# Optimization experiments

Hardware: AMD Instinct MI355X
Metric: run time of the kernel (lower is better)

The kernel has to match this reference:

```python
import jax, jax.numpy as jnp
import numpy as np

BN_EPS = 1e-5


def setup_inputs() -> dict:
    key = jax.random.key(0)
    k1, k2, k3 = jax.random.split(key, 3)
    B, C, H, W = 8, 1024, 48, 48
    Cb = 512
    x = jax.random.normal(k1, (B, C, H, W), dtype=jnp.float32)
    Wg = jax.random.normal(k2, (Cb, C), dtype=jnp.float32) * (1.0 / np.sqrt(C))
    Wz = jax.random.normal(k3, (C, Cb), dtype=jnp.float32) * (1.0 / np.sqrt(Cb))
    gamma = jnp.zeros((C,), dtype=jnp.float32)  # BN weight, const-init 0
    beta = jnp.zeros((C,), dtype=jnp.float32)   # BN bias,  const-init 0
    return {"x": x, "Wg": Wg, "Wz": Wz, "gamma": gamma, "beta": beta}


def reference(x, Wg, Wz, gamma, beta):
    B, C, H, W = x.shape
    HW = H * W
    xf = x.reshape(B, C, HW)                                  # [B,C,N]
    # attn[b,n,m] = <x[b,:,n], x[b,:,m]> / (H*W), softmax over m
    attn = jnp.einsum('bcn,bcm->bnm', xf, xf) / HW            # [B,N,N]
    attn = jax.nn.softmax(attn, axis=-1)
    # g: 1x1 conv C -> Cb (no bias)
    g = jnp.einsum('dc,bcn->bdn', Wg, xf)                     # [B,Cb,N]
    # y[b,d,n] = sum_m attn[b,n,m] * g[b,d,m]
    y = jnp.einsum('bnm,bdm->bdn', attn, g)                   # [B,Cb,N]
    # W_z: 1x1 conv Cb -> C (no bias)
    wy = jnp.einsum('cd,bdn->bcn', Wz, y)                     # [B,C,N]
    # BatchNorm2d in training mode: batch stats over (B, N), biased variance
    mean = jnp.mean(wy, axis=(0, 2), keepdims=True)
    var = jnp.mean(jnp.square(wy - mean), axis=(0, 2), keepdims=True)
    wy_bn = (wy - mean) * jax.lax.rsqrt(var + BN_EPS)
    wy_bn = wy_bn * gamma[None, :, None] + beta[None, :, None]
    z = wy_bn.reshape(B, C, H, W) + x
    return z
```

## Files before the change

### kernel.cpp

```cpp
#include <hip/hip_runtime.h>
#include <hip/hip_bf16.h>
#include <stdint.h>


typedef __bf16 bf16;
typedef __attribute__((ext_vector_type(8))) __bf16 bf16x8;
typedef __attribute__((ext_vector_type(4))) float f32x4;

template <bool F32OUT, bool BNRED>
__global__ __launch_bounds__(256)
void gemm_bt(const bf16* __restrict__ Ag, const bf16* __restrict__ Bg,
             void* __restrict__ Dg, int K, int N,
             long long sA, long long sB, long long sD, float alpha,
             float* __restrict__ ps, float* __restrict__ pq)
{
    __shared__ char lds[32768];
    char* ldsA = lds;
    char* ldsB = lds + 16384;

    const int lane = threadIdx.x & 63;
    const int wv   = threadIdx.x >> 6;
    const int wm   = wv >> 1;
    const int wn   = wv & 1;

    const bf16* Ab = Ag + (long long)blockIdx.z * sA + (long long)blockIdx.y * 128 * K;
    const bf16* Bb = Bg + (long long)blockIdx.z * sB + (long long)blockIdx.x * 128 * K;

    f32x4 acc[4][4];
    #pragma unroll
    for (int i = 0; i < 4; ++i)
        #pragma unroll
        for (int j = 0; j < 4; ++j) {
            f32x4 z = {0.f, 0.f, 0.f, 0.f};
            acc[i][j] = z;
        }

    for (int k0 = 0; k0 < K; k0 += 64) {
        #pragma unroll
        for (int t = 0; t < 4; ++t) {
            int ch  = (wv * 4 + t) * 64 + lane;
            int row = ch >> 3;
            int cc  = (ch & 7) ^ (row & 7);
            bf16x8 va = *(const bf16x8*)(Ab + (long long)row * K + k0 + cc * 8);
            bf16x8 vb = *(const bf16x8*)(Bb + (long long)row * K + k0 + cc * 8);
            *(bf16x8*)(ldsA + ch * 16) = va;
            *(bf16x8*)(ldsB + ch * 16) = vb;
        }
        __syncthreads();

        #pragma unroll
        for (int kk = 0; kk < 64; kk += 32) {
            bf16x8 af[4], bfr[4];
            #pragma unroll
            for (int i = 0; i < 4; ++i) {
                int r = wm * 64 + i * 16 + (lane & 15);
                int c = ((kk >> 3) + (lane >> 4)) ^ (r & 7);
                af[i] = *(const bf16x8*)(ldsA + r * 128 + c * 16);
            }
            #pragma unroll
            for (int j = 0; j < 4; ++j) {
                int r = wn * 64 + j * 16 + (lane & 15);
                int c = ((kk >> 3) + (lane >> 4)) ^ (r & 7);
                bfr[j] = *(const bf16x8*)(ldsB + r * 128 + c * 16);
            }
            #pragma unroll
            for (int i = 0; i < 4; ++i)
                #pragma unroll
                for (int j = 0; j < 4; ++j)
                    acc[i][j] = __builtin_amdgcn_mfma_f32_16x16x32_bf16(af[i], bfr[j], acc[i][j], 0, 0, 0);
        }
        __syncthreads();
    }

    float* bs = (float*)lds;
    float* bq = (float*)(lds + 512);
    if (BNRED) {
        if (threadIdx.x < 128) { bs[threadIdx.x] = 0.f; bq[threadIdx.x] = 0.f; }
        __syncthreads();
    }

    const int m_base = blockIdx.y * 128 + wm * 64;
    const int n_base = blockIdx.x * 128 + wn * 64;
    float s_it[4][4], q_it[4][4];
    #pragma unroll
    for (int i = 0; i < 4; ++i) {
        #pragma unroll
        for (int t = 0; t < 4; ++t) { s_it[i][t] = 0.f; q_it[i][t] = 0.f; }
    }
    #pragma unroll
    for (int i = 0; i < 4; ++i) {
        #pragma unroll
        for (int j = 0; j < 4; ++j) {
            int col = n_base + j * 16 + (lane & 15);
            #pragma unroll
            for (int t = 0; t < 4; ++t) {
                int rowg = m_base + i * 16 + (lane >> 4) * 4 + t;
                float v = acc[i][j][t] * alpha;
                if (F32OUT) ((float*)Dg)[(long long)blockIdx.z * sD + (long long)rowg * N + col] = v;
                else        ((bf16*)Dg)[(long long)blockIdx.z * sD + (long long)rowg * N + col] = (bf16)v;
                if (BNRED) { s_it[i][t] += v; q_it[i][t] += v * v; }
            }
        }
    }

    if (BNRED) {
        #pragma unroll
        for (int i = 0; i < 4; ++i) {
            #pragma unroll
            for (int t = 0; t < 4; ++t) {
                float s = s_it[i][t], q = q_it[i][t];
                #pragma unroll
                for (int m = 1; m < 16; m <<= 1) {
                    s += __shfl_xor(s, m);
                    q += __shfl_xor(q, m);
                }
                if ((lane & 15) == 0) {
                    int cl = wm * 64 + i * 16 + (lane >> 4) * 4 + t;
                    atomicAdd(&bs[cl], s);
                    atomicAdd(&bq[cl], q);
                }
            }
        }
        __syncthreads();
        if (threadIdx.x < 128) {
            int cg = blockIdx.y * 128 + threadIdx.x;
            atomicAdd(&ps[cg], bs[threadIdx.x]);
            atomicAdd(&pq[cg], bq[threadIdx.x]);
        }
    }
}

__global__ __launch_bounds__(256)
void f32_to_bf16(const float* __restrict__ in, bf16* __restrict__ out, int n)
{
    int idx = (blockIdx.x * 256 + threadIdx.x) * 4;
    if (idx < n) {
        float4 v = *(const float4*)(in + idx);
        out[idx + 0] = (bf16)v.x;
        out[idx + 1] = (bf16)v.y;
        out[idx + 2] = (bf16)v.z;
        out[idx + 3] = (bf16)v.w;
    }
}

__global__ __launch_bounds__(256)
void zero_f32(float* __restrict__ p)
{
    p[blockIdx.x * 256 + threadIdx.x] = 0.f;
}

__global__ __launch_bounds__(256)
void transpose_f32_bf16(const float* __restrict__ x, bf16* __restrict__ xT)
{
    __shared__ bf16 tile[32][33];
    const float* xb = x + (long long)blockIdx.z * 1024 * 2304;
    bf16* xo = xT + (long long)blockIdx.z * 2304 * 1024;
    const int n0 = blockIdx.x * 32;
    const int c0 = blockIdx.y * 32;
    const int tx = threadIdx.x, ty = threadIdx.y;
    #pragma unroll
    for (int i = 0; i < 32; i += 8)
        tile[ty + i][tx] = (bf16)xb[(long long)(c0 + ty + i) * 2304 + n0 + tx];
    __syncthreads();
    #pragma unroll
    for (int i = 0; i < 32; i += 8)
        xo[(long long)(n0 + ty + i) * 1024 + c0 + tx] = tile[tx][ty + i];
}

__global__ __launch_bounds__(256)
void softmax_rows(bf16* __restrict__ S)
{
    bf16* p = S + (long long)blockIdx.x * 2304;
    const int t = threadIdx.x;
    __shared__ float red[256];

    bf16x8 v8 = *(const bf16x8*)(p + t * 8);
    float vt = (float)p[2048 + t];
    float f[8];
    float mx = vt;
    #pragma unroll
    for (int i = 0; i < 8; ++i) { f[i] = (float)v8[i]; mx = fmaxf(mx, f[i]); }

    red[t] = mx; __syncthreads();
    for (int s = 128; s > 0; s >>= 1) { if (t < s) red[t] = fmaxf(red[t], red[t + s]); __syncthreads(); }
    mx = red[0];
    __syncthreads();

    float sum = 0.f;
    #pragma unroll
    for (int i = 0; i < 8; ++i) { f[i] = __expf(f[i] - mx); sum += f[i]; }
    vt = __expf(vt - mx); sum += vt;

    red[t] = sum; __syncthreads();
    for (int s = 128; s > 0; s >>= 1) { if (t < s) red[t] += red[t + s]; __syncthreads(); }
    float inv = 1.0f / red[0];

    bf16x8 o;
    #pragma unroll
    for (int i = 0; i < 8; ++i) o[i] = (bf16)(f[i] * inv);
    *(bf16x8*)(p + t * 8) = o;
    p[2048 + t] = (bf16)(vt * inv);
}

__global__ __launch_bounds__(256)
void bn_finalize(const float* __restrict__ ps, const float* __restrict__ pq,
                 float* __restrict__ mean, float* __restrict__ istd)
{
    int c = blockIdx.x * 256 + threadIdx.x;
    float mu = ps[c] / 18432.0f;
    mean[c] = mu;
    istd[c] = rsqrtf(pq[c] / 18432.0f - mu * mu + 1e-5f);
}

__global__ __launch_bounds__(256)
void bn_apply(const float* __restrict__ wy, const float* __restrict__ x,
              const float* __restrict__ gamma, const float* __restrict__ beta,
              const float* __restrict__ mean, const float* __restrict__ istd,
              float* __restrict__ z)
{
    long long idx = ((long long)blockIdx.x * 256 + threadIdx.x) * 4;
    int c = (int)((idx / 2304) & 1023);
    float sc = gamma[c] * istd[c];
    float sh = beta[c] - mean[c] * sc;
    float4 w  = *(const float4*)(wy + idx);
    float4 xv = *(const float4*)(x + idx);
    float4 o;
    o.x = w.x * sc + sh + xv.x;
    o.y = w.y * sc + sh + xv.y;
    o.z = w.z * sc + sh + xv.z;
    o.w = w.w * sc + sh + xv.w;
    *(float4*)(z + idx) = o;
}

extern "C" void kernel_launch(void* const* d_in, const int* in_sizes, int n_in,
                              void* d_out, int out_size, void* d_ws, size_t ws_size,
                              hipStream_t stream)
{
    const float* x     = (const float*)d_in[0];
    const float* Wg    = (const float*)d_in[1];
    const float* Wz    = (const float*)d_in[2];
    const float* gamma = (const float*)d_in[3];
    const float* beta  = (const float*)d_in[4];
    float* zo = (float*)d_out;

    const int B = 8, C = 1024, Cb = 512, N = 2304;

    const size_t fixedB = ((size_t)Cb * C * 2) * 2 + (size_t)C * 4 * 4 + 4096;
    const size_t perB   = ((size_t)N * C + (size_t)Cb * N + (size_t)N * N + (size_t)N * Cb) * 2 + 1024;
    int BC = 8;
    while (BC > 1 && fixedB + perB * (size_t)BC > ws_size) BC >>= 1;

    char* p = (char*)d_ws;
    auto alloc = [&](size_t bytes) { char* r = p; p += (bytes + 255) & ~(size_t)255; return r; };
    bf16*  Wgb  = (bf16*)alloc((size_t)Cb * C * 2);
    bf16*  Wzb  = (bf16*)alloc((size_t)C * Cb * 2);
    float* psum = (float*)alloc((size_t)C * 4);
    float* pqsm = (float*)alloc((size_t)C * 4);
    float* mean = (float*)alloc((size_t)C * 4);
    float* istd = (float*)alloc((size_t)C * 4);
    bf16*  xT   = (bf16*)alloc((size_t)BC * N * C * 2);
    bf16*  g    = (bf16*)alloc((size_t)BC * Cb * N * 2);
    bf16*  attn = (bf16*)alloc((size_t)BC * N * N * 2);
    bf16*  yT   = (bf16*)alloc((size_t)BC * N * Cb * 2);

    f32_to_bf16<<<dim3((Cb * C) / (256 * 4)), 256, 0, stream>>>(Wg, Wgb, Cb * C);
    f32_to_bf16<<<dim3((C * Cb) / (256 * 4)), 256, 0, stream>>>(Wz, Wzb, C * Cb);
    zero_f32<<<dim3(8), 256, 0, stream>>>(psum);

    for (int cs = 0; cs < B; cs += BC) {
        const float* xc = x + (long long)cs * C * N;
        float* wyc = zo + (long long)cs * C * N;

        transpose_f32_bf16<<<dim3(N / 32, C / 32, BC), dim3(32, 8), 0, stream>>>(xc, xT);

        gemm_bt<false, false><<<dim3(N / 128, Cb / 128, BC), 256, 0, stream>>>(
            Wgb, xT, g, C, N, 0, (long long)N * C, (long long)Cb * N, 1.0f, nullptr, nullptr);

        gemm_bt<false, false><<<dim3(N / 128, N / 128, BC), 256, 0, stream>>>(
            xT, xT, attn, C, N, (long long)N * C, (long long)N * C, (long long)N * N, 1.0f / 2304.0f,
            nullptr, nullptr);

        softmax_rows<<<dim3(BC * N), 256, 0, stream>>>(attn);

        gemm_bt<false, false><<<dim3(Cb / 128, N / 128, BC), 256, 0, stream>>>(
            attn, g, yT, N, Cb, (long long)N * N, (long long)Cb * N, (long long)N * Cb, 1.0f,
            nullptr, nullptr);

        gemm_bt<true, true><<<dim3(N / 128, C / 128, BC), 256, 0, stream>>>(
            Wzb, yT, wyc, Cb, N, 0, (long long)N * Cb, (long long)C * N, 1.0f, psum, pqsm);
    }

    bn_finalize<<<dim3(C / 256), 256, 0, stream>>>(psum, pqsm, mean, istd);
    bn_apply<<<dim3((B * C * N) / (256 * 4)), 256, 0, stream>>>(zo, x, gamma, beta, mean, istd, zo);
}
```

Before: 445.0 us.

## Add 256x256-tile 8-wave GEMM with double-buffered LDS pipeline for bf16 GEMMs

Adds a new bf16 GEMM kernel using 256x256 output tiles with 512 threads, XOR-swizzled LDS, a 128-wide K step split into phases, register-staged global prefetch into a double-buffered 128KB LDS, and s_setprio around MFMA bursts. It replaces the 128x128 kernel for the g, attention and attn*g GEMMs. The larger tiles are meant to raise arithmetic intensity and overlap global loads with MFMA work. In exchange they reduce grid size, which may hurt occupancy and CU fill for the smaller GEMMs. They also need heavy LDS and register use and assume dimensions divisible by 256.

New measurement: 458.3 us. 3.0% more time.

```diff
diff --git a/kernel.cpp b/kernel.cpp
--- a/kernel.cpp
+++ b/kernel.cpp
@@ -6,6 +6,157 @@
 typedef __bf16 bf16;
 typedef __attribute__((ext_vector_type(8))) __bf16 bf16x8;
 typedef __attribute__((ext_vector_type(4))) float f32x4;
+
+__device__ __forceinline__ void wg_barrier()
+{
+    asm volatile("" ::: "memory");
+    __builtin_amdgcn_s_barrier();
+    asm volatile("" ::: "memory");
+}
+
+__global__ __launch_bounds__(512, 2)
+void gemm_bt256(const bf16* __restrict__ Ag, const bf16* __restrict__ Bg,
+                bf16* __restrict__ Dg, int K, int N,
+                long long sA, long long sB, long long sD, float alpha)
+{
+    __shared__ __align__(16) char lds[131072];
+
+    const int tid  = threadIdx.x;
+    const int lane = tid & 63;
+    const int wv   = tid >> 6;
+    const int wm   = wv >> 2;
+    const int wn   = wv & 3;
+
+    const bf16* Ab = Ag + (long long)blockIdx.z * sA + (long long)blockIdx.y * 256 * K;
+    const bf16* Bb = Bg + (long long)blockIdx.z * sB + (long long)blockIdx.x * 256 * K;
+
+    const int r0 = tid >> 3,        c0 = (tid & 7) ^ (r0 & 7);
+    const int r1 = (tid + 512) >> 3, c1 = (tid & 7) ^ (r1 & 7);
+    auto gofs0 = [&](int half, int kb) { return (half * 128 + r0) * K + kb + c0 * 8; };
+    auto gofs1 = [&](int half, int kb) { return (half * 128 + r1) * K + kb + c1 * 8; };
+
+    const int NIT = K >> 7;
+
+    static constexpr int  srcB[8] = {1, 1, 0, 0, 1, 1, 0, 0};
+    static constexpr int  half[8] = {0, 1, 0, 1, 0, 1, 0, 1};
+    static constexpr int  kof [8] = {128, 128, 128, 128, 192, 192, 192, 192};
+    static constexpr int  wof [8] = {98304, 114688, 65536, 81920, 32768, 49152, 0, 16384};
+
+    f32x4 acc[8][4];
+    #pragma unroll
+    for (int i = 0; i < 8; ++i)
+        #pragma unroll
+        for (int j = 0; j < 4; ++j) {
+            f32x4 z = {0.f, 0.f, 0.f, 0.f};
+            acc[i][j] = z;
+        }
+
+    bf16x8 sl[4][2];
+    bf16x8 bfrag[4][2];
+
+    {
+        bf16x8 b0a = *(const bf16x8*)(Bb + gofs0(0, 0));
+        bf16x8 b0b = *(const bf16x8*)(Bb + gofs1(0, 0));
+        bf16x8 b1a = *(const bf16x8*)(Bb + gofs0(1, 0));
+        bf16x8 b1b = *(const bf16x8*)(Bb + gofs1(1, 0));
+        bf16x8 a0a = *(const bf16x8*)(Ab + gofs0(0, 0));
+        bf16x8 a0b = *(const bf16x8*)(Ab + gofs1(0, 0));
+        bf16x8 a1a = *(const bf16x8*)(Ab + gofs0(1, 0));
+        bf16x8 a1b = *(const bf16x8*)(Ab + gofs1(1, 0));
+        sl[0][0] = *(const bf16x8*)(Bb + gofs0(0, 64));
+        sl[0][1] = *(const bf16x8*)(Bb + gofs1(0, 64));
+        sl[1][0] = *(const bf16x8*)(Bb + gofs0(1, 64));
+        sl[1][1] = *(const bf16x8*)(Bb + gofs1(1, 64));
+        sl[2][0] = *(const bf16x8*)(Ab + gofs0(0, 64));
+        sl[2][1] = *(const bf16x8*)(Ab + gofs1(0, 64));
+        sl[3][0] = *(const bf16x8*)(Ab + gofs0(1, 64));
+        sl[3][1] = *(const bf16x8*)(Ab + gofs1(1, 64));
+        *(bf16x8*)(lds + 32768 + tid * 16) = b0a;
+        *(bf16x8*)(lds + 40960 + tid * 16) = b0b;
+        *(bf16x8*)(lds + 49152 + tid * 16) = b1a;
+        *(bf16x8*)(lds + 57344 + tid * 16) = b1b;
+        *(bf16x8*)(lds + 0     + tid * 16) = a0a;
+        *(bf16x8*)(lds + 8192  + tid * 16) = a0b;
+        *(bf16x8*)(lds + 16384 + tid * 16) = a1a;
+        *(bf16x8*)(lds + 24576 + tid * 16) = a1b;
+        asm volatile("s_waitcnt lgkmcnt(0)" ::: "memory");
+        wg_barrier();
+        __builtin_amdgcn_sched_barrier(0);
+    }
+
+    for (int it = 0; it < NIT; ++it) {
+        const int kc = it << 7;
+        const bool pf = (it + 1 < NIT);
+        #pragma unroll
+        for (int p = 0; p < 8; ++p) {
+            const int d = p >> 2, q = p & 3, s = p & 3;
+            char* dA = lds + d * 65536;
+            char* dB = dA + 32768;
+
+            if (q == 0) {
+                #pragma unroll
+                for (int j = 0; j < 4; ++j) {
+                    int r = wn * 64 + j * 16 + (lane & 15);
+                    #pragma unroll
+                    for (int ks = 0; ks < 2; ++ks) {
+                        int c = ((ks * 4) + (lane >> 4)) ^ (r & 7);
+                        bfrag[j][ks] = *(const bf16x8*)(dB + r * 128 + c * 16);
+                    }
+                }
+            }
+            bf16x8 af[2][2];
+            #pragma unroll
+            for (int ii = 0; ii < 2; ++ii) {
+                int r = wm * 128 + (q * 2 + ii) * 16 + (lane & 15);
+                #pragma unroll
+                for (int ks = 0; ks < 2; ++ks) {
+                    int c = ((ks * 4) + (lane >> 4)) ^ (r & 7);
+                    af[ii][ks] = *(const bf16x8*)(dA + r * 128 + c * 16);
+                }
+            }
+
+            if (p < 4 || pf) {
+                *(bf16x8*)(lds + wof[p] + tid * 16)        = sl[s][0];
+                *(bf16x8*)(lds + wof[p] + 8192 + tid * 16) = sl[s][1];
+            }
+            if (pf) {
+                const bf16* src = srcB[p] ? Bb : Ab;
+                sl[s][0] = *(const bf16x8*)(src + gofs0(half[p], kc + kof[p]));
+                sl[s][1] = *(const bf16x8*)(src + gofs1(half[p], kc + kof[p]));
+            }
+
+            wg_barrier();
+            asm volatile("s_waitcnt lgkmcnt(0)" ::: "memory");
+            __builtin_amdgcn_s_setprio(1);
+            #pragma unroll
+            for (int ks = 0; ks < 2; ++ks)
+                #pragma unroll
+                for (int ii = 0; ii < 2; ++ii)
+                    #pragma unroll
+                    for (int j = 0; j < 4; ++j)
+                        acc[q * 2 + ii][j] = __builtin_amdgcn_mfma_f32_16x16x32_bf16(
+                            af[ii][ks], bfrag[j][ks], acc[q * 2 + ii][j], 0, 0, 0);
+            __builtin_amdgcn_s_setprio(0);
+            wg_barrier();
+            __builtin_amdgcn_sched_barrier(0);
+        }
+    }
+
+    const int m_base = blockIdx.y * 256 + wm * 128;
+    const int n_base = blockIdx.x * 256 + wn * 64;
+    bf16* Db = Dg + (long long)blockIdx.z * sD;
+    #pragma unroll
+    for (int i = 0; i < 8; ++i)
+        #pragma unroll
+        for (int j = 0; j < 4; ++j) {
+            int col = n_base + j * 16 + (lane & 15);
+            #pragma unroll
+            for (int t = 0; t < 4; ++t) {
+                int rowg = m_base + i * 16 + (lane >> 4) * 4 + t;
+                Db[(long long)rowg * N + col] = (bf16)(acc[i][j][t] * alpha);
+            }
+        }
+}
 
 template <bool F32OUT, bool BNRED>
 __global__ __launch_bounds__(256)
@@ -273,18 +424,17 @@
 
         transpose_f32_bf16<<<dim3(N / 32, C / 32, BC), dim3(32, 8), 0, stream>>>(xc, xT);
 
-        gemm_bt<false, false><<<dim3(N / 128, Cb / 128, BC), 256, 0, stream>>>(
-            Wgb, xT, g, C, N, 0, (long long)N * C, (long long)Cb * N, 1.0f, nullptr, nullptr);
-
-        gemm_bt<false, false><<<dim3(N / 128, N / 128, BC), 256, 0, stream>>>(
-            xT, xT, attn, C, N, (long long)N * C, (long long)N * C, (long long)N * N, 1.0f / 2304.0f,
-            nullptr, nullptr);
+        gemm_bt256<<<dim3(N / 256, Cb / 256, BC), 512, 0, stream>>>(
+            Wgb, xT, g, C, N, 0, (long long)N * C, (long long)Cb * N, 1.0f);
+
+        gemm_bt256<<<dim3(N / 256, N / 256, BC), 512, 0, stream>>>(
+            xT, xT, attn, C, N, (long long)N * C, (long long)N * C, (long long)N * N,
+            1.0f / 2304.0f);
 
         softmax_rows<<<dim3(BC * N), 256, 0, stream>>>(attn);
 
-        gemm_bt<false, false><<<dim3(Cb / 128, N / 128, BC), 256, 0, stream>>>(
-            attn, g, yT, N, Cb, (long long)N * N, (long long)Cb * N, (long long)N * Cb, 1.0f,
-            nullptr, nullptr);
+        gemm_bt256<<<dim3(Cb / 256, N / 256, BC), 512, 0, stream>>>(
+            attn, g, yT, N, Cb, (long long)N * N, (long long)Cb * N, (long long)N * Cb, 1.0f);
 
         gemm_bt<true, true><<<dim3(N / 128, C / 128, BC), 256, 0, stream>>>(
             Wzb, yT, wyc, Cb, N, 0, (long long)N * Cb, (long long)C * N, 1.0f, psum, pqsm);
```

## Exploit symmetry of x^T x to compute only upper-triangular attention tiles

Applied to the files above, without the earlier changes.

Replaces the attention-score GEMM with a kernel that computes only tiles on or above the diagonal, since x^T x is symmetric. Off-diagonal tiles also write their transpose through an LDS staging buffer, and diagonal tiles load the operand only once. This roughly halves the matmul work for the largest GEMM. In exchange, half the launched blocks exit immediately, scalar LDS transpose writes are added, and LDS use grows slightly.

After: 436.0 us. 1.02x faster.

```diff
diff --git a/kernel.cpp b/kernel.cpp
--- a/kernel.cpp
+++ b/kernel.cpp
@@ -131,6 +131,105 @@
 }
 
 __global__ __launch_bounds__(256)
+void gemm_sym(const bf16* __restrict__ Xg, bf16* __restrict__ Dg,
+              int K, int N, long long sX, long long sD, float alpha)
+{
+    const int bi = blockIdx.y, bj = blockIdx.x;
+    if (bj < bi) return;
+    const bool mir  = (bj > bi);
+    const bool diag = (bj == bi);
+
+    __shared__ __align__(16) char lds[34816];
+    char* ldsA = lds;
+    char* ldsB = diag ? lds : (lds + 16384);
+
+    const int lane = threadIdx.x & 63;
+    const int wv   = threadIdx.x >> 6;
+    const int wm   = wv >> 1;
+    const int wn   = wv & 1;
+
+    const bf16* Ab = Xg + (long long)blockIdx.z * sX + (long long)bi * 128 * K;
+    const bf16* Bb = Xg + (long long)blockIdx.z * sX + (long long)bj * 128 * K;
+
+    f32x4 acc[4][4];
+    #pragma unroll
+    for (int i = 0; i < 4; ++i)
+        #pragma unroll
+        for (int j = 0; j < 4; ++j) {
+            f32x4 z = {0.f, 0.f, 0.f, 0.f};
+            acc[i][j] = z;
+        }
+
+    for (int k0 = 0; k0 < K; k0 += 64) {
+        #pragma unroll
+        for (int t = 0; t < 4; ++t) {
+            int ch  = (wv * 4 + t) * 64 + lane;
+            int row = ch >> 3;
+            int cc  = (ch & 7) ^ (row & 7);
+            bf16x8 va = *(const bf16x8*)(Ab + (long long)row * K + k0 + cc * 8);
+            *(bf16x8*)(ldsA + ch * 16) = va;
+            if (!diag) {
+                bf16x8 vb = *(const bf16x8*)(Bb + (long long)row * K + k0 + cc * 8);
+                *(bf16x8*)(ldsB + ch * 16) = vb;
+            }
+        }
+        __syncthreads();
+
+        #pragma unroll
+        for (int kk = 0; kk < 64; kk += 32) {
+            bf16x8 af[4], bfr[4];
+            #pragma unroll
+            for (int i = 0; i < 4; ++i) {
+                int r = wm * 64 + i * 16 + (lane & 15);
+                int c = ((kk >> 3) + (lane >> 4)) ^ (r & 7);
+                af[i] = *(const bf16x8*)(ldsA + r * 128 + c * 16);
+            }
+            #pragma unroll
+            for (int j = 0; j < 4; ++j) {
+                int r = wn * 64 + j * 16 + (lane & 15);
+                int c = ((kk >> 3) + (lane >> 4)) ^ (r & 7);
+                bfr[j] = *(const bf16x8*)(ldsB + r * 128 + c * 16);
+            }
+            #pragma unroll
+            for (int i = 0; i < 4; ++i)
+                #pragma unroll
+                for (int j = 0; j < 4; ++j)
+                    acc[i][j] = __builtin_amdgcn_mfma_f32_16x16x32_bf16(af[i], bfr[j], acc[i][j], 0, 0, 0);
+        }
+        __syncthreads();
+    }
+
+    bf16* Db = Dg + (long long)blockIdx.z * sD;
+    bf16 (*tr)[136] = (bf16(*)[136])lds;
+
+    #pragma unroll
+    for (int i = 0; i < 4; ++i) {
+        #pragma unroll
+        for (int j = 0; j < 4; ++j) {
+            int c_loc = wn * 64 + j * 16 + (lane & 15);
+            int col   = bj * 128 + c_loc;
+            #pragma unroll
+            for (int t = 0; t < 4; ++t) {
+                int r_loc = wm * 64 + i * 16 + (lane >> 4) * 4 + t;
+                float v = acc[i][j][t] * alpha;
+                Db[(long long)(bi * 128 + r_loc) * N + col] = (bf16)v;
+                if (mir) tr[c_loc][r_loc] = (bf16)v;
+            }
+        }
+    }
+
+    if (mir) {
+        __syncthreads();
+        const int cc = threadIdx.x >> 1, hf = threadIdx.x & 1;
+        const bf16* src = &tr[cc][hf * 64];
+        bf16* dst = Db + (long long)(bj * 128 + cc) * N + bi * 128 + hf * 64;
+        #pragma unroll
+        for (int j2 = 0; j2 < 8; ++j2)
+            *(bf16x8*)(dst + j2 * 8) = *(const bf16x8*)(src + j2 * 8);
+    }
+}
+
+__global__ __launch_bounds__(256)
 void f32_to_bf16(const float* __restrict__ in, bf16* __restrict__ out, int n)
 {
     int idx = (blockIdx.x * 256 + threadIdx.x) * 4;
@@ -276,9 +375,8 @@
         gemm_bt<false, false><<<dim3(N / 128, Cb / 128, BC), 256, 0, stream>>>(
             Wgb, xT, g, C, N, 0, (long long)N * C, (long long)Cb * N, 1.0f, nullptr, nullptr);
 
-        gemm_bt<false, false><<<dim3(N / 128, N / 128, BC), 256, 0, stream>>>(
-            xT, xT, attn, C, N, (long long)N * C, (long long)N * C, (long long)N * N, 1.0f / 2304.0f,
-            nullptr, nullptr);
+        gemm_sym<<<dim3(N / 128, N / 128, BC), 256, 0, stream>>>(
+            xT, attn, C, N, (long long)N * C, (long long)N * N, 1.0f / 2304.0f);
 
         softmax_rows<<<dim3(BC * N), 256, 0, stream>>>(attn);
 
```
